# Optimization experiments

Measured on AMD Instinct MI355X. Metric: run time of the kernel, lower is better.

The kernel has to match this reference:

```python
import jax, jax.numpy as jnp
import numpy as np

N, E, D, ED, H = 50000, 800000, 128, 16, 1
EPS = 1e-5


def setup_inputs() -> dict:
    key = jax.random.key(0)
    ks = jax.random.split(key, 12)
    return {
        "x": jax.random.normal(ks[0], (N, D), jnp.float32),
        "edge_index": jax.random.randint(ks[1], (2, E), 0, N),
        "edge_attr": jax.random.normal(ks[2], (E, ED), jnp.float32),
        # GATv2Conv params
        "W_l": jax.random.normal(ks[3], (D, H * D), jnp.float32) / np.sqrt(D),
        "b_l": jnp.zeros((H * D,), jnp.float32),
        "W_r": jax.random.normal(ks[4], (D, H * D), jnp.float32) / np.sqrt(D),
        "b_r": jnp.zeros((H * D,), jnp.float32),
        "W_e": jax.random.normal(ks[5], (ED, H * D), jnp.float32) / np.sqrt(ED),
        "att": jax.random.normal(ks[6], (H, D), jnp.float32) * 0.1,
        "bias_gat": jnp.zeros((D,), jnp.float32),
        # block params
        "weight1": jax.random.normal(ks[7], (2,), jnp.float32),
        "bn1_gamma": jnp.ones((D,), jnp.float32),
        "bn1_beta": jnp.zeros((D,), jnp.float32),
        "conv_w": jax.random.normal(ks[8], (D, D, 3), jnp.float32) / np.sqrt(3 * D),
        "conv_b": jnp.zeros((D,), jnp.float32),
        "weight2": jax.random.normal(ks[9], (2,), jnp.float32),
        "bn2_gamma": jnp.ones((D,), jnp.float32),
        "bn2_beta": jnp.zeros((D,), jnp.float32),
    }


def _batch_norm(z, gamma, beta):
    # NodeLevelBatchNorm in training mode: stats over all nodes of the batch graph
    mu = z.mean(axis=0)
    var = z.var(axis=0)
    return (z - mu) * jax.lax.rsqrt(var + EPS) * gamma + beta


def _gatv2(x, edge_index, edge_attr, W_l, b_l, W_r, b_r, W_e, att, bias_gat):
    n = x.shape[0]
    # add self loops with edge_attr fill_value=0
    loop = jnp.arange(n)
    src = jnp.concatenate([edge_index[0], loop])  # message sources j
    dst = jnp.concatenate([edge_index[1], loop])  # message targets i
    x_l = (x @ W_l + b_l).reshape(n, H, D)
    x_r = (x @ W_r + b_r).reshape(n, H, D)
    e = (edge_attr @ W_e).reshape(-1, H, D)
    e = jnp.concatenate([e, jnp.zeros((n, H, D), e.dtype)], axis=0)  # zeros: lin_edge(0)=0
    # [E+N, H, D] edge messages
    m = jax.nn.leaky_relu(x_l[src] + x_r[dst] + e, negative_slope=0.2)
    logits = jnp.einsum('ehc,hc->eh', m, att)  # [E+N, H]
    # softmax grouped by target node (every node has a self loop -> no empty segments)
    lmax = jax.ops.segment_max(logits, dst, num_segments=n)
    p = jnp.exp(logits - lmax[dst])
    denom = jax.ops.segment_sum(p, dst, num_segments=n)
    alpha = p / denom[dst]
    out = jax.ops.segment_sum(alpha[:, :, None] * x_l[src], dst, num_segments=n)  # [N,H,D]
    return out.mean(axis=1) + bias_gat  # concat=False -> head mean


def reference(x, edge_index, edge_attr, W_l, b_l, W_r, b_r, W_e, att, bias_gat,
              weight1, bn1_gamma, bn1_beta, conv_w, conv_b, weight2,
              bn2_gamma, bn2_beta):
    attn_feat = _gatv2(x, edge_index, edge_attr, W_l, b_l, W_r, b_r, W_e, att, bias_gat)
    w1 = jax.nn.softmax(weight1)
    z = w1[0] * x + w1[1] * attn_feat
    z = _batch_norm(z, bn1_gamma, bn1_beta)
    # Conv1d over the node dimension: [1, C, N] -> [1, C, N]
    z1 = jax.lax.conv_general_dilated(
        z.T[None], conv_w, window_strides=(1,), padding=[(1, 1)],
        dimension_numbers=('NCH', 'OIH', 'NCH'))
    z1 = z1[0].T + conv_b  # [N, C]
    z1 = jax.nn.leaky_relu(z1, negative_slope=0.01)  # dropout inactive in eval
    w2 = jax.nn.softmax(weight2)
    z = w2[0] * z + w2[1] * z1
    z = _batch_norm(z, bn2_gamma, bn2_beta)
    return z
```

## Files before the change

kernel.cpp:

```cpp
#include <hip/hip_runtime.h>
#include <hip/hip_bf16.h>
#include <math.h>

#define DD 128
#define EPSBN 1e-5f

typedef float f2 __attribute__((ext_vector_type(2)));

__device__ __forceinline__ float4 f4_add(float4 a, float4 b) {
    return make_float4(a.x + b.x, a.y + b.y, a.z + b.z, a.w + b.w);
}
__device__ __forceinline__ float4 f4_fma(float a, float4 b, float4 c) {
    c.x = fmaf(a, b.x, c.x); c.y = fmaf(a, b.y, c.y);
    c.z = fmaf(a, b.z, c.z); c.w = fmaf(a, b.w, c.w);
    return c;
}
__device__ __forceinline__ float leakyf(float v, float s) { return v > 0.f ? v : s * v; }

__device__ __forceinline__ unsigned short f2bf(float f) {
    unsigned u = __float_as_uint(f);
    return (unsigned short)((u + 0x7fffu + ((u >> 16) & 1u)) >> 16);
}
__device__ __forceinline__ f2 bfu2f2(unsigned u) {
    f2 r;
    r.x = __uint_as_float(u << 16);
    r.y = __uint_as_float(u & 0xFFFF0000u);
    return r;
}
__device__ __forceinline__ f2 leaky2(f2 v, float s) {
    f2 z = (f2)0.f;
    return __builtin_elementwise_max(v, z) + s * __builtin_elementwise_min(v, z);
}

__global__ __launch_bounds__(256) void k_prep(const float* __restrict__ conv_w, float* __restrict__ wT,
                                              int* __restrict__ counts, float* __restrict__ stats,
                                              int n, int nstats) {
    int idx = blockIdx.x * 256 + threadIdx.x;
    if (idx < 3 * 128 * 128) {
        int k = idx >> 14;
        int r = idx & 16383;
        int ci = r >> 7, co = r & 127;
        wT[idx] = conv_w[(size_t)co * 384 + ci * 3 + k];
    }
    int z = idx - 3 * 128 * 128;
    if (z >= 0) {
        if (z < n) counts[z] = 0;
        else if (z - n < nstats) stats[z - n] = 0.f;
    }
}

__global__ __launch_bounds__(256) void k_gemm_xlxr(
    const float* __restrict__ x, const float* __restrict__ Wl, const float* __restrict__ bl,
    const float* __restrict__ Wr, const float* __restrict__ br,
    float* __restrict__ XR, unsigned short* __restrict__ XLh, int n)
{
    __shared__ float As[64 * 33];
    __shared__ float Bs[32 * 256];
    int tid = threadIdx.x;
    int r0 = blockIdx.x * 64;
    int tx = tid & 31, ty = tid >> 5;

    float4 accL[8], accR[8];
    #pragma unroll
    for (int j = 0; j < 8; ++j) {
        accL[j] = make_float4(0.f, 0.f, 0.f, 0.f);
        accR[j] = make_float4(0.f, 0.f, 0.f, 0.f);
    }

    for (int k0 = 0; k0 < 128; k0 += 32) {
        for (int idx = tid; idx < 64 * 32; idx += 256) {
            int lrow = idx >> 5, kk = idx & 31;
            int g = r0 + lrow;
            As[lrow * 33 + kk] = (g < n) ? x[(size_t)g * DD + k0 + kk] : 0.f;
        }
        for (int idx = tid; idx < 2048; idx += 256) {
            int kk = idx >> 6, co4 = idx & 63;
            float4 v;
            if (co4 < 32) v = ((const float4*)Wl)[(size_t)(k0 + kk) * 32 + co4];
            else          v = ((const float4*)Wr)[(size_t)(k0 + kk) * 32 + (co4 - 32)];
            ((float4*)Bs)[kk * 64 + co4] = v;
        }
        __syncthreads();

        #pragma unroll 4
        for (int kk = 0; kk < 32; ++kk) {
            float a[8];
            #pragma unroll
            for (int j = 0; j < 8; ++j) a[j] = As[(ty * 8 + j) * 33 + kk];
            float4 bL = ((float4*)Bs)[kk * 64 + tx];
            float4 bR = ((float4*)Bs)[kk * 64 + 32 + tx];
            #pragma unroll
            for (int j = 0; j < 8; ++j) {
                accL[j] = f4_fma(a[j], bL, accL[j]);
                accR[j] = f4_fma(a[j], bR, accR[j]);
            }
        }
        __syncthreads();
    }

    float4 blv = ((const float4*)bl)[tx];
    float4 brv = ((const float4*)br)[tx];
    #pragma unroll
    for (int j = 0; j < 8; ++j) {
        int row = r0 + ty * 8 + j;
        if (row < n) {
            float4 L4 = f4_add(accL[j], blv);
            ((float4*)(XR + (size_t)row * DD))[tx] = f4_add(accR[j], brv);
            uint2 hp;
            hp.x = (unsigned)f2bf(L4.x) | ((unsigned)f2bf(L4.y) << 16);
            hp.y = (unsigned)f2bf(L4.z) | ((unsigned)f2bf(L4.w) << 16);
            ((uint2*)(XLh + (size_t)row * DD))[tx] = hp;
        }
    }
}

__global__ __launch_bounds__(256) void k_hist(const int* __restrict__ dst, int* __restrict__ counts, int e) {
    int idx = blockIdx.x * 256 + threadIdx.x;
    if (idx < e) atomicAdd(&counts[dst[idx]], 1);
}

__global__ __launch_bounds__(256) void k_scan1(const int* __restrict__ counts,
                                               int* __restrict__ offsets, int* __restrict__ bsum, int n) {
    __shared__ int tmp[256];
    int t = threadIdx.x;
    int i = blockIdx.x * 256 + t;
    int v = (i < n) ? counts[i] : 0;
    tmp[t] = v;
    __syncthreads();
    for (int off = 1; off < 256; off <<= 1) {
        int u = (t >= off) ? tmp[t - off] : 0;
        __syncthreads();
        tmp[t] += u;
        __syncthreads();
    }
    if (i < n) offsets[i] = tmp[t] - v;
    if (t == 255) bsum[blockIdx.x] = tmp[255];
}

__global__ __launch_bounds__(1024) void k_scan2(int* __restrict__ bsum, int nchunks) {
    __shared__ int tmp[1024];
    int t = threadIdx.x;
    int v = (t < nchunks) ? bsum[t] : 0;
    tmp[t] = v;
    __syncthreads();
    for (int off = 1; off < 1024; off <<= 1) {
        int u = (t >= off) ? tmp[t - off] : 0;
        __syncthreads();
        tmp[t] += u;
        __syncthreads();
    }
    if (t < nchunks) bsum[t] = tmp[t] - v;
    if (t == 0) bsum[nchunks] = tmp[nchunks - 1];
}

__global__ __launch_bounds__(256) void k_scan3(int* __restrict__ offsets, int* __restrict__ cursor,
                                               const int* __restrict__ bsum, int n, int nchunks) {
    int i = blockIdx.x * 256 + threadIdx.x;
    if (i < n) {
        int o = offsets[i] + bsum[i >> 8];
        offsets[i] = o;
        cursor[i] = o;
    }
    if (i == n) offsets[n] = bsum[nchunks];
}

__global__ __launch_bounds__(256) void k_scatter(const int* __restrict__ src, const int* __restrict__ dst,
                                                 int* __restrict__ cursor, int2* __restrict__ epair, int e) {
    int idx = blockIdx.x * 256 + threadIdx.x;
    if (idx >= e) return;
    int d = dst[idx];
    int pos = atomicAdd(&cursor[d], 1);
    epair[pos] = make_int2(idx, src[idx]);
}


#define EPROJ(EB_, J_, EV_) {                                                   \
    const float4* e4_ = ((const float4*)(EB_)) + (J_) * 4;                      \
    float4 a0_ = e4_[0], a1_ = e4_[1], a2_ = e4_[2], a3_ = e4_[3];              \
    f2 v_ = (f2)0.f;                                                            \
    v_ = __builtin_elementwise_fma((f2)a0_.x, w2[0],  v_);                      \
    v_ = __builtin_elementwise_fma((f2)a0_.y, w2[1],  v_);                      \
    v_ = __builtin_elementwise_fma((f2)a0_.z, w2[2],  v_);                      \
    v_ = __builtin_elementwise_fma((f2)a0_.w, w2[3],  v_);                      \
    v_ = __builtin_elementwise_fma((f2)a1_.x, w2[4],  v_);                      \
    v_ = __builtin_elementwise_fma((f2)a1_.y, w2[5],  v_);                      \
    v_ = __builtin_elementwise_fma((f2)a1_.z, w2[6],  v_);                      \
    v_ = __builtin_elementwise_fma((f2)a1_.w, w2[7],  v_);                      \
    v_ = __builtin_elementwise_fma((f2)a2_.x, w2[8],  v_);                      \
    v_ = __builtin_elementwise_fma((f2)a2_.y, w2[9],  v_);                      \
    v_ = __builtin_elementwise_fma((f2)a2_.z, w2[10], v_);                      \
    v_ = __builtin_elementwise_fma((f2)a2_.w, w2[11], v_);                      \
    v_ = __builtin_elementwise_fma((f2)a3_.x, w2[12], v_);                      \
    v_ = __builtin_elementwise_fma((f2)a3_.y, w2[13], v_);                      \
    v_ = __builtin_elementwise_fma((f2)a3_.z, w2[14], v_);                      \
    v_ = __builtin_elementwise_fma((f2)a3_.w, w2[15], v_);                      \
    EV_ = v_; }

#define GAT_LOAD4(q_, U0_, U1_, U2_, U3_, AV_) {                                \
    int2 g0_ = epair[q_], g1_ = epair[(q_) + 1];                                \
    int2 g2_ = epair[(q_) + 2], g3_ = epair[(q_) + 3];                          \
    int s0_ = __builtin_amdgcn_readfirstlane(g0_.y);                            \
    int s1_ = __builtin_amdgcn_readfirstlane(g1_.y);                            \
    int s2_ = __builtin_amdgcn_readfirstlane(g2_.y);                            \
    int s3_ = __builtin_amdgcn_readfirstlane(g3_.y);                            \
    U0_ = XLu[(size_t)s0_ * 64 + lane];                                         \
    U1_ = XLu[(size_t)s1_ * 64 + lane];                                         \
    U2_ = XLu[(size_t)s2_ * 64 + lane];                                         \
    U3_ = XLu[(size_t)s3_ * 64 + lane];                                         \
    int ej_ = esel == 0 ? g0_.x : esel == 1 ? g1_.x : esel == 2 ? g2_.x : g3_.x;\
    AV_ = edge_attr[(size_t)ej_ * 16 + ek]; }

#define GAT_COMPUTE4(U0_, U1_, U2_, U3_, EB_) {                                 \
    f2 x0_ = bfu2f2(U0_), x1_ = bfu2f2(U1_);                                    \
    f2 x2_ = bfu2f2(U2_), x3_ = bfu2f2(U3_);                                    \
    f2 ev0_, ev1_, ev2_, ev3_;                                                  \
    EPROJ(EB_, 0, ev0_); EPROJ(EB_, 1, ev1_);                                   \
    EPROJ(EB_, 2, ev2_); EPROJ(EB_, 3, ev3_);                                   \
    f2 m0_ = leaky2(x0_ + xr2 + ev0_, 0.2f);                                    \
    f2 m1_ = leaky2(x1_ + xr2 + ev1_, 0.2f);                                    \
    f2 m2_ = leaky2(x2_ + xr2 + ev2_, 0.2f);                                    \
    f2 m3_ = leaky2(x3_ + xr2 + ev3_, 0.2f);                                    \
    float l0_ = m0_.x * att2.x + m0_.y * att2.y;                                \
    float l1_ = m1_.x * att2.x + m1_.y * att2.y;                                \
    float l2_ = m2_.x * att2.x + m2_.y * att2.y;                                \
    float l3_ = m3_.x * att2.x + m3_.y * att2.y;                                \
    _Pragma("unroll")                                                           \
    for (int off_ = 32; off_ > 0; off_ >>= 1) {                                 \
        l0_ += __shfl_xor(l0_, off_, 64);                                       \
        l1_ += __shfl_xor(l1_, off_, 64);                                       \
        l2_ += __shfl_xor(l2_, off_, 64);                                       \
        l3_ += __shfl_xor(l3_, off_, 64);                                       \
    }                                                                           \
    float g0_ = __expf(l0_), g1_ = __expf(l1_);                                 \
    float g2_ = __expf(l2_), g3_ = __expf(l3_);                                 \
    S += (g0_ + g1_) + (g2_ + g3_);                                             \
    axy = __builtin_elementwise_fma((f2)g0_, x0_, axy);                         \
    axy = __builtin_elementwise_fma((f2)g1_, x1_, axy);                         \
    axy = __builtin_elementwise_fma((f2)g2_, x2_, axy);                         \
    axy = __builtin_elementwise_fma((f2)g3_, x3_, axy); }

__global__ __launch_bounds__(256) void k_gat(
    const unsigned short* __restrict__ XLh, const float* __restrict__ XR,
    const float* __restrict__ x,
    const int2* __restrict__ epair, const int* __restrict__ offsets,
    const float* __restrict__ edge_attr, const float* __restrict__ We,
    const float* __restrict__ att, const float* __restrict__ bias_gat,
    const float* __restrict__ weight1, float* __restrict__ Z,
    float* __restrict__ p1, float* __restrict__ q1, int n, int nwaves)
{
    __shared__ float ebuf[4][2][64];
    __shared__ f2 brs[4][64];
    __shared__ f2 brq[4][64];
    int wv   = threadIdx.x >> 6;
    int wid  = blockIdx.x * 4 + wv;
    int lane = threadIdx.x & 63;
    int c = lane * 2;
    int esel = lane >> 4, ek = lane & 15;
    const unsigned* __restrict__ XLu = (const unsigned*)XLh;
    float* ebA = &ebuf[wv][0][0];
    float* ebB = &ebuf[wv][1][0];

    f2 w2[16];
    #pragma unroll
    for (int k = 0; k < 16; ++k) w2[k] = *(const f2*)(We + k * DD + c);
    f2 att2 = *(const f2*)(att + c);
    f2 bg   = *(const f2*)(bias_gat + c);
    float w0 = weight1[0], w1v = weight1[1];
    float mw = fmaxf(w0, w1v);
    float e0w = __expf(w0 - mw), e1w = __expf(w1v - mw);
    float winv = 1.f / (e0w + e1w);
    float w1x = e0w * winv, w1a = e1w * winv;

    f2 bns = (f2)0.f, bnq = (f2)0.f;

    for (int i = wid; i < n; i += nwaves) {
        f2 xr2 = *(const f2*)(XR + (size_t)i * DD + c);
        f2 xli = bfu2f2(XLu[(size_t)i * 64 + lane]);

        f2 ms = leaky2(xli + xr2, 0.2f);
        float sl = ms.x * att2.x + ms.y * att2.y;
        #pragma unroll
        for (int off = 32; off > 0; off >>= 1) sl += __shfl_xor(sl, off, 64);
        float gs = __expf(sl);
        float S = gs;
        f2 axy = gs * xli;

        int p  = __builtin_amdgcn_readfirstlane(offsets[i]);
        int pe = __builtin_amdgcn_readfirstlane(offsets[i + 1]);
        int cnt = pe - p;
        int ng = cnt >> 2;

        if (ng > 0) {
            unsigned uA0, uA1, uA2, uA3, uB0, uB1, uB2, uB3;
            float avA, avB;
            GAT_LOAD4(p, uA0, uA1, uA2, uA3, avA);
            ebA[lane] = avA;
            int t = 0;
            for (;;) {
                bool mA = (t + 1 < ng);
                if (mA) GAT_LOAD4(p + 4 * (t + 1), uB0, uB1, uB2, uB3, avB);
                GAT_COMPUTE4(uA0, uA1, uA2, uA3, ebA);
                if (mA) ebB[lane] = avB;
                if (++t >= ng) break;
                bool mB = (t + 1 < ng);
                if (mB) GAT_LOAD4(p + 4 * (t + 1), uA0, uA1, uA2, uA3, avA);
                GAT_COMPUTE4(uB0, uB1, uB2, uB3, ebB);
                if (mB) ebA[lane] = avA;
                if (++t >= ng) break;
            }
        }
        for (int q = p + (ng << 2); q < pe; ++q) {
            int2 ej = epair[q];
            int eid = __builtin_amdgcn_readfirstlane(ej.x);
            int srn = __builtin_amdgcn_readfirstlane(ej.y);
            unsigned u = XLu[(size_t)srn * 64 + lane];
            const float* pa = edge_attr + (size_t)eid * 16;
            f2 ev = (f2)0.f;
            #pragma unroll
            for (int k = 0; k < 16; ++k) ev = __builtin_elementwise_fma((f2)pa[k], w2[k], ev);
            f2 x0 = bfu2f2(u);
            f2 m = leaky2(x0 + xr2 + ev, 0.2f);
            float l = m.x * att2.x + m.y * att2.y;
            #pragma unroll
            for (int off = 32; off > 0; off >>= 1) l += __shfl_xor(l, off, 64);
            float g = __expf(l);
            S += g;
            axy = __builtin_elementwise_fma((f2)g, x0, axy);
        }

        float rl = 1.f / S;
        f2 av = axy * rl + bg;
        f2 xv = *(const f2*)(x + (size_t)i * DD + c);
        f2 zv = w1x * xv + w1a * av;
        *(f2*)(Z + (size_t)i * DD + c) = zv;
        bns += zv;
        bnq = __builtin_elementwise_fma(zv, zv, bnq);
    }

    brs[wv][lane] = bns;
    brq[wv][lane] = bnq;
    __syncthreads();
    if (threadIdx.x < 64) {
        f2 s = brs[0][lane] + brs[1][lane] + brs[2][lane] + brs[3][lane];
        f2 q = brq[0][lane] + brq[1][lane] + brq[2][lane] + brq[3][lane];
        int base = (blockIdx.x & 31) * 128 + c;
        atomicAdd(&p1[base], s.x); atomicAdd(&p1[base + 1], s.y);
        atomicAdd(&q1[base], q.x); atomicAdd(&q1[base + 1], q.y);
    }
}

__global__ __launch_bounds__(128) void k_bn_finish(const float* __restrict__ sums, const float* __restrict__ sumsq,
                                                   const float* __restrict__ gamma, const float* __restrict__ beta,
                                                   float* __restrict__ scale, float* __restrict__ shift,
                                                   int n, int nparts) {
    int t = threadIdx.x;
    if (t >= 128) return;
    float s = 0.f, q = 0.f;
    for (int pp = 0; pp < nparts; ++pp) {
        s += sums[pp * 128 + t];
        q += sumsq[pp * 128 + t];
    }
    float fn = (float)n;
    float mu = s / fn;
    float var = q / fn - mu * mu;
    float rstd = rsqrtf(var + EPSBN);
    float sc = gamma[t] * rstd;
    scale[t] = sc;
    shift[t] = fmaf(-mu, sc, beta[t]);
}

__global__ __launch_bounds__(512) void k_conv(
    const float* __restrict__ Z, const float* __restrict__ scale1, const float* __restrict__ shift1,
    const float* __restrict__ wT, const float* __restrict__ conv_b,
    const float* __restrict__ weight2, float* __restrict__ Z2,
    float* __restrict__ sums2, float* __restrict__ sumsq2, int n)
{
    __shared__ float As[66 * 20];
    __shared__ float Bs[3 * 16 * 128];
    int tid = threadIdx.x;
    int r0 = blockIdx.x * 64;
    int tx = tid & 31, ty = tid >> 5;
    int rbase = ty * 4;

    float4 acc[4];
    #pragma unroll
    for (int j = 0; j < 4; ++j) acc[j] = make_float4(0.f, 0.f, 0.f, 0.f);

    for (int ci0 = 0; ci0 < 128; ci0 += 16) {
        if (tid < 264) {
            int lrow = tid >> 2, c4 = (tid & 3) * 4;
            int g = r0 - 1 + lrow;
            int cc = ci0 + c4;
            float4 v = make_float4(0.f, 0.f, 0.f, 0.f);
            if (g >= 0 && g < n) {
                float4 zv = *(const float4*)(Z + (size_t)g * DD + cc);
                const float4 s4v = *(const float4*)(scale1 + cc);
                const float4 h4v = *(const float4*)(shift1 + cc);
                v.x = fmaf(zv.x, s4v.x, h4v.x); v.y = fmaf(zv.y, s4v.y, h4v.y);
                v.z = fmaf(zv.z, s4v.z, h4v.z); v.w = fmaf(zv.w, s4v.w, h4v.w);
            }
            *(float4*)(As + lrow * 20 + c4) = v;
        }
        #pragma unroll
        for (int s = 0; s < 3; ++s) {
            int idx = s * 512 + tid;
            int k = idx >> 9;
            int r = idx & 511;
            int ci = r >> 5, co4 = r & 31;
            ((float4*)Bs)[idx] = ((const float4*)wT)[(size_t)k * 4096 + (ci0 + ci) * 32 + co4];
        }
        __syncthreads();

        #pragma unroll 2
        for (int ci = 0; ci < 16; ++ci) {
            float a[6];
            #pragma unroll
            for (int j = 0; j < 6; ++j) a[j] = As[(rbase + j) * 20 + ci];
            float4 b0 = ((float4*)Bs)[(0 * 16 + ci) * 32 + tx];
            float4 b1 = ((float4*)Bs)[(1 * 16 + ci) * 32 + tx];
            float4 b2 = ((float4*)Bs)[(2 * 16 + ci) * 32 + tx];
            #pragma unroll
            for (int j = 0; j < 4; ++j) {
                acc[j] = f4_fma(a[j],     b0, acc[j]);
                acc[j] = f4_fma(a[j + 1], b1, acc[j]);
                acc[j] = f4_fma(a[j + 2], b2, acc[j]);
            }
        }
        __syncthreads();
    }

    float w0 = weight2[0], w1v = weight2[1];
    float mw = fmaxf(w0, w1v);
    float e0 = __expf(w0 - mw), e1 = __expf(w1v - mw);
    float winv = 1.f / (e0 + e1);
    float w2x = e0 * winv, w2a = e1 * winv;

    float4 cb = ((const float4*)conv_b)[tx];
    float4 sc1 = ((const float4*)scale1)[tx];
    float4 sh1 = ((const float4*)shift1)[tx];
    float4 s4 = make_float4(0.f, 0.f, 0.f, 0.f), q4 = s4;
    #pragma unroll
    for (int j = 0; j < 4; ++j) {
        int row = r0 + rbase + j;
        if (row >= n) break;
        float4 z1 = f4_add(acc[j], cb);
        z1.x = leakyf(z1.x, 0.01f); z1.y = leakyf(z1.y, 0.01f);
        z1.z = leakyf(z1.z, 0.01f); z1.w = leakyf(z1.w, 0.01f);
        float4 zv = ((const float4*)(Z + (size_t)row * DD))[tx];
        float4 zbn;
        zbn.x = fmaf(zv.x, sc1.x, sh1.x); zbn.y = fmaf(zv.y, sc1.y, sh1.y);
        zbn.z = fmaf(zv.z, sc1.z, sh1.z); zbn.w = fmaf(zv.w, sc1.w, sh1.w);
        float4 o;
        o.x = w2x * zbn.x + w2a * z1.x; o.y = w2x * zbn.y + w2a * z1.y;
        o.z = w2x * zbn.z + w2a * z1.z; o.w = w2x * zbn.w + w2a * z1.w;
        ((float4*)(Z2 + (size_t)row * DD))[tx] = o;
        s4 = f4_add(s4, o);
        q4.x = fmaf(o.x, o.x, q4.x); q4.y = fmaf(o.y, o.y, q4.y);
        q4.z = fmaf(o.z, o.z, q4.z); q4.w = fmaf(o.w, o.w, q4.w);
    }

    float4* rs = (float4*)Bs;
    float4* rq = rs + 512;
    rs[ty * 32 + tx] = s4;
    rq[ty * 32 + tx] = q4;
    __syncthreads();
    if (tid < 32) {
        float4 ts = rs[tid], tq = rq[tid];
        #pragma unroll
        for (int j = 1; j < 16; ++j) { ts = f4_add(ts, rs[j * 32 + tid]); tq = f4_add(tq, rq[j * 32 + tid]); }
        atomicAdd(&sums2[tid * 4 + 0], ts.x); atomicAdd(&sums2[tid * 4 + 1], ts.y);
        atomicAdd(&sums2[tid * 4 + 2], ts.z); atomicAdd(&sums2[tid * 4 + 3], ts.w);
        atomicAdd(&sumsq2[tid * 4 + 0], tq.x); atomicAdd(&sumsq2[tid * 4 + 1], tq.y);
        atomicAdd(&sumsq2[tid * 4 + 2], tq.z); atomicAdd(&sumsq2[tid * 4 + 3], tq.w);
    }
}

__global__ __launch_bounds__(256) void k_final(const float* __restrict__ Z2,
                                               const float* __restrict__ scale2, const float* __restrict__ shift2,
                                               float* __restrict__ out, int total4) {
    int idx = blockIdx.x * 256 + threadIdx.x;
    if (idx >= total4) return;
    int c4 = idx & 31;
    float4 v = ((const float4*)Z2)[idx];
    float4 sc = ((const float4*)scale2)[c4];
    float4 sh = ((const float4*)shift2)[c4];
    float4 r;
    r.x = fmaf(v.x, sc.x, sh.x); r.y = fmaf(v.y, sc.y, sh.y);
    r.z = fmaf(v.z, sc.z, sh.z); r.w = fmaf(v.w, sc.w, sh.w);
    ((float4*)out)[idx] = r;
}

extern "C" void kernel_launch(void* const* d_in, const int* in_sizes, int n_in,
                              void* d_out, int out_size, void* d_ws, size_t ws_size,
                              hipStream_t stream)
{
    const float* x          = (const float*)d_in[0];
    const int*   edge_index = (const int*)d_in[1];
    const float* edge_attr  = (const float*)d_in[2];
    const float* W_l        = (const float*)d_in[3];
    const float* b_l        = (const float*)d_in[4];
    const float* W_r        = (const float*)d_in[5];
    const float* b_r        = (const float*)d_in[6];
    const float* W_e        = (const float*)d_in[7];
    const float* att        = (const float*)d_in[8];
    const float* bias_gat   = (const float*)d_in[9];
    const float* weight1    = (const float*)d_in[10];
    const float* bn1_gamma  = (const float*)d_in[11];
    const float* bn1_beta   = (const float*)d_in[12];
    const float* conv_w     = (const float*)d_in[13];
    const float* conv_b     = (const float*)d_in[14];
    const float* weight2    = (const float*)d_in[15];
    const float* bn2_gamma  = (const float*)d_in[16];
    const float* bn2_beta   = (const float*)d_in[17];

    int n = in_sizes[0] / DD;
    int e = in_sizes[1] / 2;
    int nchunks = (n + 255) / 256;

    float* XR = (float*)d_ws;
    float* Z  = XR + (size_t)n * DD;
    float* wT = Z + (size_t)n * DD;
    float* stats = wT + 49152;
    float* sums2 = stats + 256, *sumsq2 = stats + 384;
    float* scale1 = stats + 512, *shift1 = stats + 640;
    float* scale2 = stats + 768, *shift2 = stats + 896;
    float* p1 = stats + 1024;
    float* q1 = p1 + 4096;
    int* counts  = (int*)(q1 + 4096);
    int* offsets = counts + n;
    int* cursor  = offsets + n + 2;
    int* bsum    = cursor + n;
    int2* epair  = (int2*)(bsum + ((nchunks + 2) & ~1));
    unsigned short* XLh = (unsigned short*)(epair + e);
    float* Z2 = XR;

    const int* src = edge_index;
    const int* dst = edge_index + e;

    const int nwaves = 8192;
    const int nstats = 1024 + 8192;

    k_prep<<<(3 * 128 * 128 + n + nstats + 255) / 256, 256, 0, stream>>>(conv_w, wT, counts, stats, n, nstats);
    k_gemm_xlxr<<<(n + 63) / 64, 256, 0, stream>>>(x, W_l, b_l, W_r, b_r, XR, XLh, n);
    k_hist<<<(e + 255) / 256, 256, 0, stream>>>(dst, counts, e);
    k_scan1<<<nchunks, 256, 0, stream>>>(counts, offsets, bsum, n);
    k_scan2<<<1, 1024, 0, stream>>>(bsum, nchunks);
    k_scan3<<<(n + 256) / 256, 256, 0, stream>>>(offsets, cursor, bsum, n, nchunks);
    k_scatter<<<(e + 255) / 256, 256, 0, stream>>>(src, dst, cursor, epair, e);
    k_gat<<<nwaves / 4, 256, 0, stream>>>(XLh, XR, x, epair, offsets,
                                          edge_attr, W_e, att, bias_gat, weight1, Z,
                                          p1, q1, n, nwaves);
    k_bn_finish<<<1, 128, 0, stream>>>(p1, q1, bn1_gamma, bn1_beta, scale1, shift1, n, 32);
    k_conv<<<(n + 63) / 64, 512, 0, stream>>>(Z, scale1, shift1, wT, conv_b, weight2, Z2,
                                              sums2, sumsq2, n);
    k_bn_finish<<<1, 128, 0, stream>>>(sums2, sumsq2, bn2_gamma, bn2_beta, scale2, shift2, n, 1);
    k_final<<<(n * 32 + 255) / 256, 256, 0, stream>>>(Z2, scale2, shift2, (float*)d_out, n * 32);
}
```

Before: 553.3 us.

## Fold self-loops into CSR and process two destination nodes per wave

```diff
diff --git a/kernel.cpp b/kernel.cpp
--- a/kernel.cpp
+++ b/kernel.cpp
@@ -44,7 +44,7 @@
     }
     int z = idx - 3 * 128 * 128;
     if (z >= 0) {
-        if (z < n) counts[z] = 0;
+        if (z < n) counts[z] = 1;
         else if (z - n < nstats) stats[z - n] = 0.f;
     }
 }
@@ -154,12 +154,14 @@
 }
 
 __global__ __launch_bounds__(256) void k_scan3(int* __restrict__ offsets, int* __restrict__ cursor,
-                                               const int* __restrict__ bsum, int n, int nchunks) {
+                                               const int* __restrict__ bsum, int2* __restrict__ epair,
+                                               int n, int nchunks) {
     int i = blockIdx.x * 256 + threadIdx.x;
     if (i < n) {
         int o = offsets[i] + bsum[i >> 8];
         offsets[i] = o;
-        cursor[i] = o;
+        epair[o] = make_int2(-1, i);
+        cursor[i] = o + 1;
     }
     if (i == n) offsets[n] = bsum[nchunks];
 }
@@ -196,9 +198,12 @@
     v_ = __builtin_elementwise_fma((f2)a3_.w, w2[15], v_);                      \
     EV_ = v_; }
 
-#define GAT_LOAD4(q_, U0_, U1_, U2_, U3_, AV_) {                                \
-    int2 g0_ = epair[q_], g1_ = epair[(q_) + 1];                                \
-    int2 g2_ = epair[(q_) + 2], g3_ = epair[(q_) + 3];                          \
+#define GAT_LOAD4G(q_, PE_, U0_, U1_, U2_, U3_, AV_) {                          \
+    int q1_ = (q_) + 1 < (PE_) ? (q_) + 1 : (PE_) - 1;                          \
+    int q2_ = (q_) + 2 < (PE_) ? (q_) + 2 : (PE_) - 1;                          \
+    int q3_ = (q_) + 3 < (PE_) ? (q_) + 3 : (PE_) - 1;                          \
+    int2 g0_ = epair[q_], g1_ = epair[q1_];                                     \
+    int2 g2_ = epair[q2_], g3_ = epair[q3_];                                    \
     int s0_ = __builtin_amdgcn_readfirstlane(g0_.y);                            \
     int s1_ = __builtin_amdgcn_readfirstlane(g1_.y);                            \
     int s2_ = __builtin_amdgcn_readfirstlane(g2_.y);                            \
@@ -208,18 +213,18 @@
     U2_ = XLu[(size_t)s2_ * 64 + lane];                                         \
     U3_ = XLu[(size_t)s3_ * 64 + lane];                                         \
     int ej_ = esel == 0 ? g0_.x : esel == 1 ? g1_.x : esel == 2 ? g2_.x : g3_.x;\
-    AV_ = edge_attr[(size_t)ej_ * 16 + ek]; }
-
-#define GAT_COMPUTE4(U0_, U1_, U2_, U3_, EB_) {                                 \
+    AV_ = ej_ >= 0 ? edge_attr[(size_t)ej_ * 16 + ek] : 0.f; }
+
+#define GAT_COMPUTE4G(BQ_, PE_, U0_, U1_, U2_, U3_, EB_, S_, AXY_, XR2_) {      \
     f2 x0_ = bfu2f2(U0_), x1_ = bfu2f2(U1_);                                    \
     f2 x2_ = bfu2f2(U2_), x3_ = bfu2f2(U3_);                                    \
     f2 ev0_, ev1_, ev2_, ev3_;                                                  \
     EPROJ(EB_, 0, ev0_); EPROJ(EB_, 1, ev1_);                                   \
     EPROJ(EB_, 2, ev2_); EPROJ(EB_, 3, ev3_);                                   \
-    f2 m0_ = leaky2(x0_ + xr2 + ev0_, 0.2f);                                    \
-    f2 m1_ = leaky2(x1_ + xr2 + ev1_, 0.2f);                                    \
-    f2 m2_ = leaky2(x2_ + xr2 + ev2_, 0.2f);                                    \
-    f2 m3_ = leaky2(x3_ + xr2 + ev3_, 0.2f);                                    \
+    f2 m0_ = leaky2(x0_ + (XR2_) + ev0_, 0.2f);                                 \
+    f2 m1_ = leaky2(x1_ + (XR2_) + ev1_, 0.2f);                                 \
+    f2 m2_ = leaky2(x2_ + (XR2_) + ev2_, 0.2f);                                 \
+    f2 m3_ = leaky2(x3_ + (XR2_) + ev3_, 0.2f);                                 \
     float l0_ = m0_.x * att2.x + m0_.y * att2.y;                                \
     float l1_ = m1_.x * att2.x + m1_.y * att2.y;                                \
     float l2_ = m2_.x * att2.x + m2_.y * att2.y;                                \
@@ -231,13 +236,15 @@
         l2_ += __shfl_xor(l2_, off_, 64);                                       \
         l3_ += __shfl_xor(l3_, off_, 64);                                       \
     }                                                                           \
-    float g0_ = __expf(l0_), g1_ = __expf(l1_);                                 \
-    float g2_ = __expf(l2_), g3_ = __expf(l3_);                                 \
-    S += (g0_ + g1_) + (g2_ + g3_);                                             \
-    axy = __builtin_elementwise_fma((f2)g0_, x0_, axy);                         \
-    axy = __builtin_elementwise_fma((f2)g1_, x1_, axy);                         \
-    axy = __builtin_elementwise_fma((f2)g2_, x2_, axy);                         \
-    axy = __builtin_elementwise_fma((f2)g3_, x3_, axy); }
+    float g0_ = (BQ_) + 0 < (PE_) ? __expf(l0_) : 0.f;                          \
+    float g1_ = (BQ_) + 1 < (PE_) ? __expf(l1_) : 0.f;                          \
+    float g2_ = (BQ_) + 2 < (PE_) ? __expf(l2_) : 0.f;                          \
+    float g3_ = (BQ_) + 3 < (PE_) ? __expf(l3_) : 0.f;                          \
+    S_ += (g0_ + g1_) + (g2_ + g3_);                                            \
+    AXY_ = __builtin_elementwise_fma((f2)g0_, x0_, AXY_);                       \
+    AXY_ = __builtin_elementwise_fma((f2)g1_, x1_, AXY_);                       \
+    AXY_ = __builtin_elementwise_fma((f2)g2_, x2_, AXY_);                       \
+    AXY_ = __builtin_elementwise_fma((f2)g3_, x3_, AXY_); }
 
 __global__ __launch_bounds__(256) void k_gat(
     const unsigned short* __restrict__ XLh, const float* __restrict__ XR,
@@ -248,7 +255,7 @@
     const float* __restrict__ weight1, float* __restrict__ Z,
     float* __restrict__ p1, float* __restrict__ q1, int n, int nwaves)
 {
-    __shared__ float ebuf[4][2][64];
+    __shared__ float ebuf[4][4][64];
     __shared__ f2 brs[4][64];
     __shared__ f2 brq[4][64];
     int wv   = threadIdx.x >> 6;
@@ -257,8 +264,10 @@
     int c = lane * 2;
     int esel = lane >> 4, ek = lane & 15;
     const unsigned* __restrict__ XLu = (const unsigned*)XLh;
-    float* ebA = &ebuf[wv][0][0];
-    float* ebB = &ebuf[wv][1][0];
+    float* ebA0 = &ebuf[wv][0][0];
+    float* ebA1 = &ebuf[wv][1][0];
+    float* ebB0 = &ebuf[wv][2][0];
+    float* ebB1 = &ebuf[wv][3][0];
 
     f2 w2[16];
     #pragma unroll
@@ -273,68 +282,72 @@
 
     f2 bns = (f2)0.f, bnq = (f2)0.f;
 
-    for (int i = wid; i < n; i += nwaves) {
-        f2 xr2 = *(const f2*)(XR + (size_t)i * DD + c);
-        f2 xli = bfu2f2(XLu[(size_t)i * 64 + lane]);
-
-        f2 ms = leaky2(xli + xr2, 0.2f);
-        float sl = ms.x * att2.x + ms.y * att2.y;
-        #pragma unroll
-        for (int off = 32; off > 0; off >>= 1) sl += __shfl_xor(sl, off, 64);
-        float gs = __expf(sl);
-        float S = gs;
-        f2 axy = gs * xli;
-
-        int p  = __builtin_amdgcn_readfirstlane(offsets[i]);
-        int pe = __builtin_amdgcn_readfirstlane(offsets[i + 1]);
-        int cnt = pe - p;
-        int ng = cnt >> 2;
-
-        if (ng > 0) {
-            unsigned uA0, uA1, uA2, uA3, uB0, uB1, uB2, uB3;
-            float avA, avB;
-            GAT_LOAD4(p, uA0, uA1, uA2, uA3, avA);
-            ebA[lane] = avA;
-            int t = 0;
-            for (;;) {
-                bool mA = (t + 1 < ng);
-                if (mA) GAT_LOAD4(p + 4 * (t + 1), uB0, uB1, uB2, uB3, avB);
-                GAT_COMPUTE4(uA0, uA1, uA2, uA3, ebA);
-                if (mA) ebB[lane] = avB;
-                if (++t >= ng) break;
-                bool mB = (t + 1 < ng);
-                if (mB) GAT_LOAD4(p + 4 * (t + 1), uA0, uA1, uA2, uA3, avA);
-                GAT_COMPUTE4(uB0, uB1, uB2, uB3, ebB);
-                if (mB) ebA[lane] = avA;
-                if (++t >= ng) break;
-            }
-        }
-        for (int q = p + (ng << 2); q < pe; ++q) {
-            int2 ej = epair[q];
-            int eid = __builtin_amdgcn_readfirstlane(ej.x);
-            int srn = __builtin_amdgcn_readfirstlane(ej.y);
-            unsigned u = XLu[(size_t)srn * 64 + lane];
-            const float* pa = edge_attr + (size_t)eid * 16;
-            f2 ev = (f2)0.f;
-            #pragma unroll
-            for (int k = 0; k < 16; ++k) ev = __builtin_elementwise_fma((f2)pa[k], w2[k], ev);
-            f2 x0 = bfu2f2(u);
-            f2 m = leaky2(x0 + xr2 + ev, 0.2f);
-            float l = m.x * att2.x + m.y * att2.y;
-            #pragma unroll
-            for (int off = 32; off > 0; off >>= 1) l += __shfl_xor(l, off, 64);
-            float g = __expf(l);
-            S += g;
-            axy = __builtin_elementwise_fma((f2)g, x0, axy);
-        }
-
-        float rl = 1.f / S;
-        f2 av = axy * rl + bg;
-        f2 xv = *(const f2*)(x + (size_t)i * DD + c);
-        f2 zv = w1x * xv + w1a * av;
-        *(f2*)(Z + (size_t)i * DD + c) = zv;
-        bns += zv;
-        bnq = __builtin_elementwise_fma(zv, zv, bnq);
+    for (int base = wid * 2; base < n; base += 2 * nwaves) {
+        int iB = base + 1;
+        bool hasB = iB < n;
+        int iBe = base + 2 <= n ? base + 2 : n;
+        int pA  = __builtin_amdgcn_readfirstlane(offsets[base]);
+        int pm  = __builtin_amdgcn_readfirstlane(offsets[base + 1]);
+        int pBe = __builtin_amdgcn_readfirstlane(offsets[iBe]);
+        int cntA = pm - pA;
+        int cntB = hasB ? pBe - pm : 0;
+        int ngA = (cntA + 3) >> 2;
+        int ngB = (cntB + 3) >> 2;
+        int ng = ngA > ngB ? ngA : ngB;
+
+        f2 xr2A = *(const f2*)(XR + (size_t)base * DD + c);
+        f2 xr2B = hasB ? *(const f2*)(XR + (size_t)iB * DD + c) : (f2)0.f;
+
+        float SA = 0.f, SB = 0.f;
+        f2 axyA = (f2)0.f, axyB = (f2)0.f;
+
+        unsigned a00, a01, a02, a03, a10, a11, a12, a13;
+        unsigned b00, b01, b02, b03, b10, b11, b12, b13;
+        float avA0, avA1, avB0, avB1;
+
+        GAT_LOAD4G(pA, pm, a00, a01, a02, a03, avA0);
+        if (ngB > 0) GAT_LOAD4G(pm, pBe, b00, b01, b02, b03, avB0);
+        ebA0[lane] = avA0;
+        if (ngB > 0) ebB0[lane] = avB0;
+
+        int t = 0;
+        for (;;) {
+            bool mA = (t + 1 < ngA), mB = (t + 1 < ngB);
+            if (mA) GAT_LOAD4G(pA + 4 * (t + 1), pm, a10, a11, a12, a13, avA1);
+            if (mB) GAT_LOAD4G(pm + 4 * (t + 1), pBe, b10, b11, b12, b13, avB1);
+            if (t < ngA) GAT_COMPUTE4G(pA + 4 * t, pm, a00, a01, a02, a03, ebA0, SA, axyA, xr2A);
+            if (mA) ebA1[lane] = avA1;
+            if (t < ngB) GAT_COMPUTE4G(pm + 4 * t, pBe, b00, b01, b02, b03, ebB0, SB, axyB, xr2B);
+            if (mB) ebB1[lane] = avB1;
+            if (++t >= ng) break;
+            mA = (t + 1 < ngA); mB = (t + 1 < ngB);
+            if (mA) GAT_LOAD4G(pA + 4 * (t + 1), pm, a00, a01, a02, a03, avA0);
+            if (mB) GAT_LOAD4G(pm + 4 * (t + 1), pBe, b00, b01, b02, b03, avB0);
+            if (t < ngA) GAT_COMPUTE4G(pA + 4 * t, pm, a10, a11, a12, a13, ebA1, SA, axyA, xr2A);
+            if (mA) ebA0[lane] = avA0;
+            if (t < ngB) GAT_COMPUTE4G(pm + 4 * t, pBe, b10, b11, b12, b13, ebB1, SB, axyB, xr2B);
+            if (mB) ebB0[lane] = avB0;
+            if (++t >= ng) break;
+        }
+
+        f2 xvA = *(const f2*)(x + (size_t)base * DD + c);
+        f2 xvB = hasB ? *(const f2*)(x + (size_t)iB * DD + c) : (f2)0.f;
+
+        float rlA = 1.f / SA;
+        f2 avA = axyA * rlA + bg;
+        f2 zvA = w1x * xvA + w1a * avA;
+        *(f2*)(Z + (size_t)base * DD + c) = zvA;
+        bns += zvA;
+        bnq = __builtin_elementwise_fma(zvA, zvA, bnq);
+
+        if (hasB) {
+            float rlB = 1.f / SB;
+            f2 avB = axyB * rlB + bg;
+            f2 zvB = w1x * xvB + w1a * avB;
+            *(f2*)(Z + (size_t)iB * DD + c) = zvB;
+            bns += zvB;
+            bnq = __builtin_elementwise_fma(zvB, zvB, bnq);
+        }
     }
 
     brs[wv][lane] = bns;
@@ -343,9 +356,9 @@
     if (threadIdx.x < 64) {
         f2 s = brs[0][lane] + brs[1][lane] + brs[2][lane] + brs[3][lane];
         f2 q = brq[0][lane] + brq[1][lane] + brq[2][lane] + brq[3][lane];
-        int base = (blockIdx.x & 31) * 128 + c;
-        atomicAdd(&p1[base], s.x); atomicAdd(&p1[base + 1], s.y);
-        atomicAdd(&q1[base], q.x); atomicAdd(&q1[base + 1], q.y);
+        int bbase = (blockIdx.x & 31) * 128 + c;
+        atomicAdd(&p1[bbase], s.x); atomicAdd(&p1[bbase + 1], s.y);
+        atomicAdd(&q1[bbase], q.x); atomicAdd(&q1[bbase + 1], q.y);
     }
 }
 
@@ -531,7 +544,7 @@
     int* cursor  = offsets + n + 2;
     int* bsum    = cursor + n;
     int2* epair  = (int2*)(bsum + ((nchunks + 2) & ~1));
-    unsigned short* XLh = (unsigned short*)(epair + e);
+    unsigned short* XLh = (unsigned short*)(epair + e + n);
     float* Z2 = XR;
 
     const int* src = edge_index;
@@ -545,7 +558,7 @@
     k_hist<<<(e + 255) / 256, 256, 0, stream>>>(dst, counts, e);
     k_scan1<<<nchunks, 256, 0, stream>>>(counts, offsets, bsum, n);
     k_scan2<<<1, 1024, 0, stream>>>(bsum, nchunks);
-    k_scan3<<<(n + 256) / 256, 256, 0, stream>>>(offsets, cursor, bsum, n, nchunks);
+    k_scan3<<<(n + 256) / 256, 256, 0, stream>>>(offsets, cursor, bsum, epair, n, nchunks);
     k_scatter<<<(e + 255) / 256, 256, 0, stream>>>(src, dst, cursor, epair, e);
     k_gat<<<nwaves / 4, 256, 0, stream>>>(XLh, XR, x, epair, offsets,
                                           edge_attr, W_e, att, bias_gat, weight1, Z,
```

Result: slower. 618.6 us (+11.8%).
